# Performance work log

Measured on AMD Instinct MI355X. Metric: run time of the kernel, lower is better.

## Reference

```python
import jax, jax.numpy as jnp
import numpy as np

WS = 8          # window_size
OWS = 12        # overlap_win_size = int(8*0.5)+8
PAD = 2         # (OWS-WS)//2
HEADS = 6
DH = 16         # dim_head
INNER = HEADS * DH  # 96
SCALE = DH ** -0.5


def rel_to_abs(x):
    # x: (b, l, m) with m = 2*r - 1
    b, l, m = x.shape
    r = (m + 1) // 2
    x = jnp.concatenate([x, jnp.zeros((b, l, 1), x.dtype)], axis=2)
    flat = x.reshape(b, l * (m + 1))
    flat = jnp.concatenate([flat, jnp.zeros((b, m - l), x.dtype)], axis=1)
    final = flat.reshape(b, l + 1, m)[:, :l, m - r:]
    return final  # (b, l, r)


def relative_logits_1d(q, rel_k):
    # q: (B, X, Y, d), rel_k: (2r-1, d)
    B, X, Y, _ = q.shape
    r = (rel_k.shape[0] + 1) // 2
    logits = jnp.einsum('bxyd,rd->bxyr', q, rel_k)           # (B, X, Y, 2r-1)
    logits = rel_to_abs(logits.reshape(B * X, Y, -1)).reshape(B, X, Y, r)
    logits = jnp.broadcast_to(logits[:, :, None], (B, X, r, Y, r))  # b x i y j
    return logits


def rel_pos_emb(q, rel_height, rel_width):
    # q: (B, WS*WS, d) -> bias (B, WS*WS, OWS*OWS)
    B, _, d = q.shape
    qg = q.reshape(B, WS, WS, d)
    lw = relative_logits_1d(qg, rel_width)                   # (B, x, i, y, j)
    lw = lw.transpose(0, 1, 3, 2, 4).reshape(B, WS * WS, OWS * OWS)  # b (x y) (i j)
    lh = relative_logits_1d(qg.transpose(0, 2, 1, 3), rel_height)    # (B, y, i, x, j) roles swapped
    lh = lh.transpose(0, 3, 1, 4, 2).reshape(B, WS * WS, OWS * OWS)  # b (y x) (j i)
    return lw + lh


def unfold_windows(t, nh, nw):
    # torch nn.Unfold(kernel=OWS, stride=WS, padding=PAD) then
    # rearrange 'b (c j) i -> (b i) j c' -> (b*nh*nw, OWS*OWS, C)
    b, C, _, _ = t.shape
    tp = jnp.pad(t, ((0, 0), (0, 0), (PAD, PAD), (PAD, PAD)))
    ridx = (jnp.arange(nh) * WS)[:, None] + jnp.arange(OWS)   # (nh, OWS)
    cidx = (jnp.arange(nw) * WS)[:, None] + jnp.arange(OWS)   # (nw, OWS)
    p = tp[:, :, ridx, :]            # (b, C, nh, OWS, Wp)
    p = p[:, :, :, :, cidx]          # (b, C, nh, OWS, nw, OWS)
    p = p.transpose(0, 2, 4, 3, 5, 1)  # (b, nh, nw, OWS, OWS, C)
    return p.reshape(b * nh * nw, OWS * OWS, C)


def split_heads(t):
    # (B, n, heads*dh) -> (B*heads, n, dh)
    B, n, _ = t.shape
    return t.reshape(B, n, HEADS, DH).transpose(0, 2, 1, 3).reshape(B * HEADS, n, DH)


def setup_inputs() -> dict:
    key = jax.random.key(0)
    k = jax.random.split(key, 5)
    x = jax.random.normal(k[0], (2, 96, 256, 256), jnp.float32)
    qkv_w = jax.random.normal(k[1], (288, 96), jnp.float32) * 0.05
    qkv_b = jnp.zeros((288,), jnp.float32)
    proj_w = jax.random.normal(k[2], (96, 96), jnp.float32) * 0.05
    proj_b = jnp.zeros((96,), jnp.float32)
    rel_height = jax.random.normal(k[3], (23, 16), jnp.float32) * SCALE
    rel_width = jax.random.normal(k[4], (23, 16), jnp.float32) * SCALE
    return {"x": x, "qkv_w": qkv_w, "qkv_b": qkv_b, "proj_w": proj_w,
            "proj_b": proj_b, "rel_height": rel_height, "rel_width": rel_width}


def reference(x, qkv_w, qkv_b, proj_w, proj_b, rel_height, rel_width):
    b, c, h, w = x.shape
    nh, nw = h // WS, w // WS
    qkv = jnp.einsum('oc,bchw->bohw', qkv_w, x) + qkv_b[None, :, None, None]
    qs, ks, vs = jnp.split(qkv, 3, axis=1)  # each (b, INNER, h, w)
    # queries: non-overlapping windows 'b c (h p1) (w p2) -> (b h w) (p1 p2) c'
    qs = qs.reshape(b, INNER, nh, WS, nw, WS).transpose(0, 2, 4, 3, 5, 1)
    qs = qs.reshape(b * nh * nw, WS * WS, INNER)
    ks = unfold_windows(ks, nh, nw)  # (b*nh*nw, OWS*OWS, INNER)
    vs = unfold_windows(vs, nh, nw)
    qs, ks, vs = map(split_heads, (qs, ks, vs))  # (B*heads, n, DH)
    qs = qs * SCALE
    attn = jnp.einsum('bqd,bkd->bqk', qs, ks)
    attn = attn + rel_pos_emb(qs, rel_height, rel_width)
    attn = jax.nn.softmax(attn, axis=-1)
    out = jnp.einsum('bqk,bkd->bqd', attn, vs)  # (b*nh*nw*heads, WS*WS, DH)
    out = out.reshape(b, nh, nw, HEADS, WS, WS, DH)
    out = out.transpose(0, 3, 6, 1, 4, 2, 5).reshape(b, INNER, h, w)
    out = jnp.einsum('oc,bchw->bohw', proj_w, out) + proj_b[None, :, None, None]
    return out
```

## Files before the change

### kernel.cpp

```cpp
#include <hip/hip_runtime.h>
#include <hip/hip_bf16.h>


typedef __attribute__((ext_vector_type(8))) short bf16x8;
typedef __attribute__((ext_vector_type(4))) float f32x4;

__device__ __forceinline__ f32x4 mfma16(bf16x8 a, bf16x8 b, f32x4 c) {
  return __builtin_amdgcn_mfma_f32_16x16x32_bf16(a, b, c, 0, 0, 0);
}
__device__ __forceinline__ short f2b(float f) {
  unsigned u = __builtin_bit_cast(unsigned, f);
  unsigned r = u + 0x7fffu + ((u >> 16) & 1u);
  return (short)(r >> 16);
}
__device__ __forceinline__ void splitf(float x, short& h, short& l) {
  unsigned u = __builtin_bit_cast(unsigned, x);
  h = (short)(u >> 16);
  float fh = __builtin_bit_cast(float, u & 0xffff0000u);
  l = f2b(x - fh);
}

#define KPLANE 1081600L

__global__ __launch_bounds__(256) void prep_kernel(
    const float* __restrict__ qkv_w, const float* __restrict__ proj_w,
    const float* __restrict__ rel_h, const float* __restrict__ rel_w,
    short* __restrict__ qwh, short* __restrict__ qwl,
    short* __restrict__ pwh, short* __restrict__ pwl,
    short* __restrict__ rhb, short* __restrict__ rwb,
    short* __restrict__ k_t) {
  int i = blockIdx.x * 256 + threadIdx.x;
  if (i < 288 * 96) {
    short h, l;
    splitf(qkv_w[i], h, l);
    qwh[i] = h;
    qwl[i] = l;
  }
  if (i < 96 * 96) {
    short h, l;
    splitf(proj_w[i], h, l);
    pwh[i] = h;
    pwl[i] = l;
  }
  if (i < 368) {
    rhb[i] = f2b(rel_h[i]);
    rwb[i] = f2b(rel_w[i]);
  }
  if (i < 12 * 2064) {
    int plane = i / 2064, r = i - plane * 2064;
    int py, px;
    if (r < 1040) {
      int rowid = r / 260;
      py = (rowid < 2) ? rowid : 256 + rowid;
      px = r - rowid * 260;
    } else {
      int r2 = r - 1040;
      py = 2 + (r2 >> 2);
      int cid = r2 & 3;
      px = (cid < 2) ? cid : 256 + cid;
    }
    bf16x8 z = {0, 0, 0, 0, 0, 0, 0, 0};
    long base = (long)plane * KPLANE + (long)(py * 260 + px) * 16;
    *(bf16x8*)(k_t + base) = z;
    *(bf16x8*)(k_t + base + 8) = z;
  }
}

__global__ __launch_bounds__(256) void qkv_kernel(
    const float* __restrict__ x, const short* __restrict__ qwh,
    const short* __restrict__ qwl, const float* __restrict__ bias,
    short* __restrict__ q_t, short* __restrict__ k_t,
    short* __restrict__ v_t) {
  __shared__ __attribute__((aligned(16))) short Ah[4][32][104];
  const int tid = threadIdx.x;
  const int wave = tid >> 6, lane = tid & 63;
  const int quad = lane >> 4, col = lane & 15;
  const long P0 = (long)blockIdx.x * 128 + wave * 32;
  const int b = (int)(P0 >> 16);
  const int hw0 = (int)(P0 & 65535);

  {
    const long base = ((long)b * 96) << 16;
    const int px0 = (lane & 7) * 4;
    for (int i = 0; i < 12; ++i) {
      int c = i * 8 + (lane >> 3);
      float4 v = *(const float4*)(x + base + ((long)c << 16) + hw0 + px0);
      Ah[wave][px0][c] = f2b(v.x);
      Ah[wave][px0 + 1][c] = f2b(v.y);
      Ah[wave][px0 + 2][c] = f2b(v.z);
      Ah[wave][px0 + 3][c] = f2b(v.w);
    }
  }
  bf16x8 af[2][3];
  for (int mt = 0; mt < 2; ++mt)
    for (int ks = 0; ks < 3; ++ks)
      af[mt][ks] = *(const bf16x8*)&Ah[wave][mt * 16 + col][ks * 32 + quad * 8];

  for (int t = 0; t < 3; ++t) {
    const float scale = (t == 0) ? 0.25f * 1.44269504f : 1.0f;
    for (int i6 = 0; i6 < 6; ++i6) {
      const int o = (t * 6 + i6) * 16 + col;
      bf16x8 bh[3], bl[3];
      for (int ks = 0; ks < 3; ++ks) {
        bh[ks] = *(const bf16x8*)(qwh + o * 96 + ks * 32 + quad * 8);
        bl[ks] = *(const bf16x8*)(qwl + o * 96 + ks * 32 + quad * 8);
      }
      float bv = bias[o];
      f32x4 acc0 = {bv, bv, bv, bv}, acc1 = acc0;
      for (int ks = 0; ks < 3; ++ks) {
        acc0 = mfma16(af[0][ks], bh[ks], acc0);
        acc0 = mfma16(af[0][ks], bl[ks], acc0);
        acc1 = mfma16(af[1][ks], bh[ks], acc1);
        acc1 = mfma16(af[1][ks], bl[ks], acc1);
      }
      for (int r = 0; r < 4; ++r) {
        Ah[wave][quad * 4 + r][i6 * 16 + col] = f2b(acc0[r] * scale);
        Ah[wave][16 + quad * 4 + r][i6 * 16 + col] = f2b(acc1[r] * scale);
      }
    }
    if (t == 1) {
      const int py = (hw0 >> 8) + 2;
      const int pxb = (hw0 & 255) + 2;
      for (int i = 0; i < 6; ++i) {
        int linear = i * 64 + lane;
        int px = linear / 12, c = linear - px * 12;
        int h = c >> 1, half = c & 1;
        bf16x8 vv = *(const bf16x8*)&Ah[wave][px][c * 8];
        *(bf16x8*)(k_t + (long)(h * 2 + b) * KPLANE +
                   (long)(py * 260 + pxb + px) * 16 + half * 8) = vv;
      }
    } else {
      short* plane0 = (t == 0) ? q_t : v_t;
      for (int i = 0; i < 6; ++i) {
        int linear = i * 64 + lane;
        int px = linear / 12, c = linear - px * 12;
        int h = c >> 1, half = c & 1;
        bf16x8 vv = *(const bf16x8*)&Ah[wave][px][c * 8];
        *(bf16x8*)(plane0 + (long)h * 2097152 + (P0 + px) * 16 + half * 8) =
            vv;
      }
    }
  }
}

__global__ __launch_bounds__(256) void attn_kernel(
    const short* __restrict__ q_t, const short* __restrict__ k_t,
    const short* __restrict__ v_t, const short* __restrict__ rhb,
    const short* __restrict__ rwb, short* __restrict__ ao) {
  __shared__ __attribute__((aligned(16))) short v_lds[16][168];
  __shared__ __attribute__((aligned(16))) char scratch[4][5120];

  const int win = blockIdx.x, head = blockIdx.y;
  const int b = win >> 10, wy = (win & 1023) >> 5, wx = win & 31;
  const int y0 = wy * 8 - 2, x0 = wx * 8 - 2;
  const long pb = (long)b << 16;
  const int tid = threadIdx.x;

  if (tid < 160) {
    const int key = tid;
    bool valid = false;
    long pix = 0;
    if (key < 144) {
      int kh = key / 12, kw = key - kh * 12;
      int gy = y0 + kh, gx = x0 + kw;
      valid = ((unsigned)gy < 256u) && ((unsigned)gx < 256u);
      pix = pb + gy * 256 + gx;
    }
    if (valid) {
      const short* src = v_t + (long)head * 2097152 + pix * 16;
      union { bf16x8 v; short s[8]; } u0, u1;
      u0.v = *(const bf16x8*)src;
      u1.v = *(const bf16x8*)(src + 8);
      for (int d = 0; d < 8; ++d) {
        v_lds[d][key] = u0.s[d];
        v_lds[d + 8][key] = u1.s[d];
      }
    } else {
      for (int d = 0; d < 16; ++d) v_lds[d][key] = 0;
    }
  }
  __syncthreads();

  const int wave = tid >> 6, lane = tid & 63;
  const int quad = lane >> 4, col = lane & 15;
  float* dWs = (float*)scratch[wave];
  float* dHt = dWs + 600;
  short* pp = (short*)scratch[wave];

  const short* qp = q_t + (long)head * 2097152;
  const short* kpb = k_t + (long)(head * 2 + b) * KPLANE;

  bf16x8 qf = {0, 0, 0, 0, 0, 0, 0, 0};
  if (quad < 2) {
    int qg = wave * 16 + col;
    int qy = qg >> 3, qx = qg & 7;
    qf = *(const bf16x8*)(qp + (pb + (wy * 8 + qy) * 256 + wx * 8 + qx) * 16 +
                          quad * 8);
  }

  for (int nt = 0; nt < 2; ++nt) {
    int r = nt * 16 + col;
    bf16x8 bw = {0, 0, 0, 0, 0, 0, 0, 0}, bh2 = bw;
    if (quad < 2 && r < 23) {
      bw = *(const bf16x8*)(rwb + r * 16 + quad * 8);
      bh2 = *(const bf16x8*)(rhb + r * 16 + quad * 8);
    }
    f32x4 z = {0.f, 0.f, 0.f, 0.f};
    f32x4 aw = mfma16(qf, bw, z);
    f32x4 ah = mfma16(qf, bh2, z);
    if (r < 23)
      for (int r4 = 0; r4 < 4; ++r4) {
        int ql = quad * 4 + r4;
        dWs[(r + (ql & 7)) * 20 + ql] = aw[r4];
        dHt[r * 20 + ql] = ah[r4];
      }
  }

  f32x4 L[9];
  {
    int kh = (col >= 12) ? 1 : 0, kw = col - 12 * kh;
    const short* ka =
        kpb + (long)((wy * 8 + kh) * 260 + wx * 8 + kw) * 16 + quad * 8;
    for (int nt = 0; nt < 9; ++nt) {
      bf16x8 kf = *(const bf16x8*)ka;
      f32x4 z = {0.f, 0.f, 0.f, 0.f};
      L[nt] = mfma16(qf, kf, z);
      kw += 4;
      if (kw >= 12) {
        kw -= 12;
        ka += 512 * 16;
      } else {
        ka += 264 * 16;
      }
    }
  }

  const int qy4 = wave * 2 + (quad >> 1);
  {
    int kh = (col >= 12) ? 1 : 0, kw = col - 12 * kh;
    for (int nt = 0; nt < 9; ++nt) {
      f32x4 wv = *(const f32x4*)&dWs[(11 + kw) * 20 + quad * 4];
      f32x4 hv = *(const f32x4*)&dHt[(11 + kh - qy4) * 20 + quad * 4];
      for (int r4 = 0; r4 < 4; ++r4)
        L[nt][r4] = __builtin_amdgcn_exp2f(L[nt][r4] + wv[r4] + hv[r4]);
      kw += 4;
      kh += 1;
      if (kw >= 12) {
        kw -= 12;
        kh += 1;
      }
    }
  }
  for (int nt = 0; nt < 9; ++nt)
    for (int r4 = 0; r4 < 4; ++r4)
      pp[(quad * 4 + r4) * 160 + nt * 16 + col] = f2b(L[nt][r4]);
  for (int r4 = 0; r4 < 4; ++r4) pp[(quad * 4 + r4) * 160 + 144 + col] = 0;

  const bf16x8 ones = {0x3F80, 0x3F80, 0x3F80, 0x3F80,
                       0x3F80, 0x3F80, 0x3F80, 0x3F80};
  f32x4 oacc = {0.f, 0.f, 0.f, 0.f}, oaccS = oacc;
  for (int ks = 0; ks < 5; ++ks) {
    bf16x8 pa = *(const bf16x8*)(pp + col * 160 + ks * 32 + quad * 8);
    bf16x8 vb = *(const bf16x8*)&v_lds[col][ks * 32 + quad * 8];
    oacc = mfma16(pa, vb, oacc);
    oaccS = mfma16(pa, ones, oaccS);
  }
  for (int r4 = 0; r4 < 4; ++r4) {
    int qg = wave * 16 + quad * 4 + r4;
    int qy = qg >> 3, qx = qg & 7;
    float val = oacc[r4] * __builtin_amdgcn_rcpf(oaccS[r4]);
    ao[(pb + (wy * 8 + qy) * 256 + wx * 8 + qx) * 96 + head * 16 + col] =
        f2b(val);
  }
}

__global__ __launch_bounds__(256) void proj_kernel(
    const short* __restrict__ ao, const short* __restrict__ pwh,
    const short* __restrict__ pwl, const float* __restrict__ bias,
    float* __restrict__ out) {
  const int tid = threadIdx.x;
  const int wave = tid >> 6, lane = tid & 63;
  const int quad = lane >> 4, col = lane & 15;
  const long P0 = (long)blockIdx.x * 128 + wave * 32;

  bf16x8 bfr[2][3];
  for (int nt = 0; nt < 2; ++nt) {
    long pix = P0 + nt * 16 + col;
    for (int ks = 0; ks < 3; ++ks)
      bfr[nt][ks] = *(const bf16x8*)(ao + pix * 96 + ks * 32 + quad * 8);
  }
  f32x4 acc[6][2];
  for (int mt = 0; mt < 6; ++mt) {
    for (int r = 0; r < 4; ++r) {
      float bv = bias[mt * 16 + quad * 4 + r];
      acc[mt][0][r] = bv;
      acc[mt][1][r] = bv;
    }
    bf16x8 afh[3], afl[3];
    for (int ks = 0; ks < 3; ++ks) {
      afh[ks] =
          *(const bf16x8*)(pwh + (mt * 16 + col) * 96 + ks * 32 + quad * 8);
      afl[ks] =
          *(const bf16x8*)(pwl + (mt * 16 + col) * 96 + ks * 32 + quad * 8);
    }
    for (int ks = 0; ks < 3; ++ks) {
      acc[mt][0] = mfma16(afh[ks], bfr[0][ks], acc[mt][0]);
      acc[mt][0] = mfma16(afl[ks], bfr[0][ks], acc[mt][0]);
      acc[mt][1] = mfma16(afh[ks], bfr[1][ks], acc[mt][1]);
      acc[mt][1] = mfma16(afl[ks], bfr[1][ks], acc[mt][1]);
    }
  }
  const int bb = (int)(P0 >> 16);
  const int hw0 = (int)(P0 & 65535);
  for (int mt = 0; mt < 6; ++mt)
    for (int nt = 0; nt < 2; ++nt)
      for (int r = 0; r < 4; ++r) {
        int o = mt * 16 + quad * 4 + r;
        int hw = hw0 + nt * 16 + col;
        out[(((long)(bb * 96 + o)) << 16) + hw] = acc[mt][nt][r];
      }
}

extern "C" void kernel_launch(void* const* d_in, const int* in_sizes, int n_in,
                              void* d_out, int out_size, void* d_ws,
                              size_t ws_size, hipStream_t stream) {
  const float* x = (const float*)d_in[0];
  const float* qkv_w = (const float*)d_in[1];
  const float* qkv_b = (const float*)d_in[2];
  const float* proj_w = (const float*)d_in[3];
  const float* proj_b = (const float*)d_in[4];
  const float* rel_h = (const float*)d_in[5];
  const float* rel_w = (const float*)d_in[6];

  const long NPIXC = 131072L * 96L;
  short* q_t = (short*)d_ws;
  short* k_t = q_t + NPIXC;
  short* v_t = k_t + 12 * KPLANE;
  short* ao = v_t + NPIXC;
  short* qwh = ao + NPIXC;
  short* qwl = qwh + 288 * 96;
  short* pwh = qwl + 288 * 96;
  short* pwl = pwh + 96 * 96;
  short* rhb = pwl + 96 * 96;
  short* rwb = rhb + 368;
  float* out = (float*)d_out;

  hipLaunchKernelGGL(prep_kernel, dim3(108), dim3(256), 0, stream, qkv_w,
                     proj_w, rel_h, rel_w, qwh, qwl, pwh, pwl, rhb, rwb, k_t);
  hipLaunchKernelGGL(qkv_kernel, dim3(1024), dim3(256), 0, stream, x, qwh, qwl,
                     qkv_b, q_t, k_t, v_t);
  hipLaunchKernelGGL(attn_kernel, dim3(2048, 6), dim3(256), 0, stream, q_t,
                     k_t, v_t, rhb, rwb, ao);
  hipLaunchKernelGGL(proj_kernel, dim3(1024), dim3(256), 0, stream, ao, pwh,
                     pwl, proj_b, out);
}
```

Before: 211.5 us.

## Pack softmax probs with cvt_pk, swizzle window order, head-planar attention output

Probabilities are now converted with packed bf16 conversion and stored transposed, key-major with padded stride, then regathered with byte-permute into MFMA A-fragments instead of scalar short stores. The block index is remapped so that consecutive blocks cover windows spread across batches and rows. The attention output moves from pixel-interleaved 96-channel layout to per-head planes, and the projection kernel's loads are changed to read that layout. This aims to cut LDS store instructions and bank conflicts and to improve L2 locality, at the cost of extra permute ALU work and strided LDS reads.

```diff
diff --git a/kernel.cpp b/kernel.cpp
--- a/kernel.cpp
+++ b/kernel.cpp
@@ -12,6 +12,11 @@
   unsigned u = __builtin_bit_cast(unsigned, f);
   unsigned r = u + 0x7fffu + ((u >> 16) & 1u);
   return (short)(r >> 16);
+}
+__device__ __forceinline__ unsigned cvtpk(float lo, float hi) {
+  unsigned r;
+  asm("v_cvt_pk_bf16_f32 %0, %1, %2" : "=v"(r) : "v"(lo), "v"(hi));
+  return r;
 }
 __device__ __forceinline__ void splitf(float x, short& h, short& l) {
   unsigned u = __builtin_bit_cast(unsigned, x);
@@ -148,9 +153,10 @@
     const short* __restrict__ v_t, const short* __restrict__ rhb,
     const short* __restrict__ rwb, short* __restrict__ ao) {
   __shared__ __attribute__((aligned(16))) short v_lds[16][168];
-  __shared__ __attribute__((aligned(16))) char scratch[4][5120];
-
-  const int win = blockIdx.x, head = blockIdx.y;
+  __shared__ __attribute__((aligned(16))) char scratch[4][5248];
+
+  const int orig = blockIdx.x, head = blockIdx.y;
+  const int win = ((orig & 7) << 8) | (orig >> 3);
   const int b = win >> 10, wy = (win & 1023) >> 5, wx = win & 31;
   const int y0 = wy * 8 - 2, x0 = wx * 8 - 2;
   const long pb = (long)b << 16;
@@ -185,7 +191,7 @@
   const int quad = lane >> 4, col = lane & 15;
   float* dWs = (float*)scratch[wave];
   float* dHt = dWs + 600;
-  short* pp = (short*)scratch[wave];
+  unsigned* ppd = (unsigned*)scratch[wave];
 
   const short* qp = q_t + (long)head * 2097152;
   const short* kpb = k_t + (long)(head * 2 + b) * KPLANE;
@@ -251,26 +257,42 @@
       }
     }
   }
-  for (int nt = 0; nt < 9; ++nt)
-    for (int r4 = 0; r4 < 4; ++r4)
-      pp[(quad * 4 + r4) * 160 + nt * 16 + col] = f2b(L[nt][r4]);
-  for (int r4 = 0; r4 < 4; ++r4) pp[(quad * 4 + r4) * 160 + 144 + col] = 0;
-
+  asm volatile("" ::: "memory");
+
+  for (int nt = 0; nt < 9; ++nt) {
+    unsigned d0 = cvtpk(L[nt][0], L[nt][1]);
+    unsigned d1 = cvtpk(L[nt][2], L[nt][3]);
+    int base = (nt * 16 + col) * 9 + quad * 2;
+    ppd[base] = d0;
+    ppd[base + 1] = d1;
+  }
+
+  const unsigned sel = (col & 1) ? 0x07060302u : 0x05040100u;
   const bf16x8 ones = {0x3F80, 0x3F80, 0x3F80, 0x3F80,
                        0x3F80, 0x3F80, 0x3F80, 0x3F80};
   f32x4 oacc = {0.f, 0.f, 0.f, 0.f}, oaccS = oacc;
   for (int ks = 0; ks < 5; ++ks) {
-    bf16x8 pa = *(const bf16x8*)(pp + col * 160 + ks * 32 + quad * 8);
+    int k0 = ks * 32 + quad * 8;
+    bool live = k0 < 144;
+    int k0c = live ? k0 : 136;
+    const unsigned* rp = ppd + k0c * 9 + (col >> 1);
+    unsigned r0 = rp[0], r1 = rp[9], r2 = rp[18], r3 = rp[27];
+    unsigned r4v = rp[36], r5 = rp[45], r6 = rp[54], r7 = rp[63];
+    union { unsigned u[4]; bf16x8 v; } pu;
+    pu.u[0] = live ? __builtin_amdgcn_perm(r1, r0, sel) : 0u;
+    pu.u[1] = live ? __builtin_amdgcn_perm(r3, r2, sel) : 0u;
+    pu.u[2] = live ? __builtin_amdgcn_perm(r5, r4v, sel) : 0u;
+    pu.u[3] = live ? __builtin_amdgcn_perm(r7, r6, sel) : 0u;
     bf16x8 vb = *(const bf16x8*)&v_lds[col][ks * 32 + quad * 8];
-    oacc = mfma16(pa, vb, oacc);
-    oaccS = mfma16(pa, ones, oaccS);
+    oacc = mfma16(pu.v, vb, oacc);
+    oaccS = mfma16(pu.v, ones, oaccS);
   }
   for (int r4 = 0; r4 < 4; ++r4) {
     int qg = wave * 16 + quad * 4 + r4;
     int qy = qg >> 3, qx = qg & 7;
     float val = oacc[r4] * __builtin_amdgcn_rcpf(oaccS[r4]);
-    ao[(pb + (wy * 8 + qy) * 256 + wx * 8 + qx) * 96 + head * 16 + col] =
-        f2b(val);
+    ao[(long)head * 2097152 +
+       (pb + (wy * 8 + qy) * 256 + wx * 8 + qx) * 16 + col] = f2b(val);
   }
 }
 
@@ -286,8 +308,11 @@
   bf16x8 bfr[2][3];
   for (int nt = 0; nt < 2; ++nt) {
     long pix = P0 + nt * 16 + col;
-    for (int ks = 0; ks < 3; ++ks)
-      bfr[nt][ks] = *(const bf16x8*)(ao + pix * 96 + ks * 32 + quad * 8);
+    for (int ks = 0; ks < 3; ++ks) {
+      int c0 = ks * 32 + quad * 8;
+      bfr[nt][ks] = *(const bf16x8*)(ao + (long)(c0 >> 4) * 2097152 +
+                                     pix * 16 + (c0 & 15));
+    }
   }
   f32x4 acc[6][2];
   for (int mt = 0; mt < 6; ++mt) {
```

Measured after the change: 200.2 us. 5.3% less time.
